# Kernel tuning notes

Hardware: AMD Instinct MI355X
Metric: run time of the kernel (lower is better)

The kernel has to match this reference:

```python
import jax, jax.numpy as jnp
import numpy as np

COST_KEYPOINT = 1.0
COST_GIOU = 1.0


def box_cxcyczwhd_to_xyzxyz(b):
    c, s = b[..., :3], b[..., 3:]
    return jnp.concatenate([c - 0.5 * s, c + 0.5 * s], axis=-1)


def generalized_3d_box_iou(b1, b2):
    # b1: [N,6], b2: [M,6], both xyzxyz. Returns [N,M] GIoU.
    vol1 = jnp.prod(b1[:, 3:] - b1[:, :3], axis=-1)
    vol2 = jnp.prod(b2[:, 3:] - b2[:, :3], axis=-1)
    lt = jnp.maximum(b1[:, None, :3], b2[None, :, :3])
    rb = jnp.minimum(b1[:, None, 3:], b2[None, :, 3:])
    inter = jnp.prod(jnp.maximum(rb - lt, 0.0), axis=-1)
    union = vol1[:, None] + vol2[None, :] - inter
    iou = inter / union
    elt = jnp.minimum(b1[:, None, :3], b2[None, :, :3])
    erb = jnp.maximum(b1[:, None, 3:], b2[None, :, 3:])
    evol = jnp.prod(jnp.maximum(erb - elt, 0.0), axis=-1)
    return iou - (evol - union) / evol


@jax.jit
def compute_cost(pred_keypoints, pred_boxes, tgt_boxes, tgt_keypoints):
    bs, Q = pred_keypoints.shape[:2]
    out_kp = pred_keypoints.reshape(bs * Q, -1)            # [bs*Q, K*3]
    out_boxes = pred_boxes.reshape(bs * Q, 6)
    tgt_b = tgt_boxes.reshape(-1, 6)                        # [T_total, 6]
    tgt_kp = tgt_keypoints.reshape(tgt_b.shape[0], -1)      # [T_total, K*3]
    xyz_min = box_cxcyczwhd_to_xyzxyz(tgt_b)[:, :3]
    K3 = tgt_kp.shape[-1]
    kp = tgt_kp.reshape(-1, K3 // 3, 3)
    # normalize keypoints relative to box min-corner and box size
    dist_kp = ((kp - xyz_min[:, None, :]) / tgt_b[:, None, 3:]).reshape(-1, K3)
    # L1 cdist: [bs*Q, T_total]
    cost_kp = jnp.sum(jnp.abs(out_kp[:, None, :] - dist_kp[None, :, :]), axis=-1)
    cost_giou = -generalized_3d_box_iou(
        box_cxcyczwhd_to_xyzxyz(out_boxes), box_cxcyczwhd_to_xyzxyz(tgt_b))
    C = COST_KEYPOINT * cost_kp + COST_GIOU * cost_giou
    return C.reshape(bs, Q, -1)


def _lap(cost):
    # Jonker-Volgenant shortest-augmenting-path LAP (scipy-style).
    # cost: [n, m] with n <= m. Returns (arange(n), col4row).
    cost = np.asarray(cost, dtype=np.float64)
    n, m = cost.shape
    u = np.zeros(n)
    v = np.zeros(m)
    col4row = np.full(n, -1, np.int64)
    row4col = np.full(m, -1, np.int64)
    for curRow in range(n):
        path = np.full(m, -1, np.int64)
        SR = np.zeros(n, bool)
        SC = np.zeros(m, bool)
        shortest = np.full(m, np.inf)
        minVal = 0.0
        i = curRow
        sink = -1
        while sink == -1:
            SR[i] = True
            idx = np.where(~SC)[0]
            r = minVal + cost[i, idx] - u[i] - v[idx]
            better = r < shortest[idx]
            shortest[idx[better]] = r[better]
            path[idx[better]] = i
            jloc = np.argmin(shortest[idx])
            j = idx[jloc]
            minVal = shortest[j]
            SC[j] = True
            if row4col[j] == -1:
                sink = j
            else:
                i = row4col[j]
        u[curRow] += minVal
        mask = SR.copy()
        mask[curRow] = False
        u[mask] += minVal - shortest[col4row[mask]]
        v[SC] -= minVal - shortest[SC]
        j = sink
        while True:
            i = path[j]
            row4col[j] = i
            col4row[i], j = j, col4row[i]
            if i == curRow:
                break
    return np.arange(n), col4row


def _linear_sum_assignment(cost):
    # cost: [Q, T] with Q >= T; mirrors scipy's transpose handling:
    # returns (row_ind sorted ascending, matching col_ind).
    rows, cols = _lap(cost.T)  # rows = arange(T) targets, cols = query ids
    order = np.argsort(cols)
    return cols[order], rows[order]


def setup_inputs() -> dict:
    key = jax.random.key(0)
    k1, k2, k3, k4, k5, k6 = jax.random.split(key, 6)
    BS, Q, T, K = 16, 300, 50, 17
    pred_keypoints = jax.random.normal(k1, (BS, Q, K * 3), dtype=jnp.float32)
    pred_boxes = jnp.concatenate([
        jax.random.uniform(k2, (BS, Q, 3), dtype=jnp.float32),
        jax.random.uniform(k3, (BS, Q, 3), dtype=jnp.float32) * 0.5 + 0.05,
    ], axis=-1)
    tgt_boxes = jnp.concatenate([
        jax.random.uniform(k4, (BS, T, 3), dtype=jnp.float32),
        jax.random.uniform(k5, (BS, T, 3), dtype=jnp.float32) * 0.5 + 0.05,
    ], axis=-1)
    tgt_keypoints = jax.random.uniform(k6, (BS, T, K * 3), dtype=jnp.float32)
    return {"pred_keypoints": pred_keypoints, "pred_boxes": pred_boxes,
            "tgt_boxes": tgt_boxes, "tgt_keypoints": tgt_keypoints}


def reference(pred_keypoints, pred_boxes, tgt_boxes, tgt_keypoints):
    C = compute_cost(pred_keypoints, pred_boxes, tgt_boxes, tgt_keypoints)
    Cn = np.asarray(C)
    bs, Q, _ = Cn.shape
    T = tgt_boxes.shape[1]
    # per-image block of the column-split cost matrix, as in torch C.split(sizes, -1)
    idx = []
    for b in range(bs):
        i, j = _linear_sum_assignment(Cn[b, :, b * T:(b + 1) * T])
        idx.append(np.stack([i, j]))
    indices = jnp.asarray(np.stack(idx), dtype=jnp.int32)  # [bs, 2, T]
    return C, indices
```

## Files before the change

kernel.cpp:

```cpp
#include <hip/hip_runtime.h>
#include <math.h>

#define BSZ 16
#define NQ 300
#define NT 50
#define K3 51
#define NPRED (BSZ*NQ)
#define NTGT  (BSZ*NT)
#define NC    (NPRED*NTGT)
#define TSTRIDE 301
#define SMEMF 15232


template<int CTRL, int RMASK>
__device__ __forceinline__ double dpp_minstep_f64(double x) {
    long long bb = __double_as_longlong(x);
    int lo = (int)(bb & 0xFFFFFFFFll);
    int hi = (int)(bb >> 32);
    int mlo = __builtin_amdgcn_update_dpp(lo, lo, CTRL, RMASK, 0xF, false);
    int mhi = __builtin_amdgcn_update_dpp(hi, hi, CTRL, RMASK, 0xF, false);
    double other = __longlong_as_double(((long long)mhi << 32) | (long long)(unsigned)mlo);
    return fmin(x, other);
}
__device__ __forceinline__ double wave_min_f64(double x) {
    x = dpp_minstep_f64<0xB1, 0xF>(x);
    x = dpp_minstep_f64<0x4E, 0xF>(x);
    x = dpp_minstep_f64<0x141, 0xF>(x);
    x = dpp_minstep_f64<0x140, 0xF>(x);
    x = dpp_minstep_f64<0x142, 0xA>(x);
    x = dpp_minstep_f64<0x143, 0xC>(x);
    long long bb = __double_as_longlong(x);
    int lo = __builtin_amdgcn_readlane((int)(bb & 0xFFFFFFFFll), 63);
    int hi = __builtin_amdgcn_readlane((int)(bb >> 32), 63);
    return __longlong_as_double(((long long)hi << 32) | (long long)(unsigned)lo);
}
__device__ __forceinline__ double readlane_f64(double x, int lane) {
    long long bb = __double_as_longlong(x);
    int lo = __builtin_amdgcn_readlane((int)(bb & 0xFFFFFFFFll), lane);
    int hi = __builtin_amdgcn_readlane((int)(bb >> 32), lane);
    return __longlong_as_double(((long long)hi << 32) | (long long)(unsigned)lo);
}

__device__ __forceinline__ float giou_cost(
    float plt0, float plt1, float plt2, float prb0, float prb1, float prb2, float pvol,
    float tlt0, float tlt1, float tlt2, float trb0, float trb1, float trb2, float tvol)
{
    float inter = fmaxf(fminf(prb0,trb0) - fmaxf(plt0,tlt0), 0.f);
    inter *= fmaxf(fminf(prb1,trb1) - fmaxf(plt1,tlt1), 0.f);
    inter *= fmaxf(fminf(prb2,trb2) - fmaxf(plt2,tlt2), 0.f);
    float evol = fmaxf(fmaxf(prb0,trb0) - fminf(plt0,tlt0), 0.f);
    evol *= fmaxf(fmaxf(prb1,trb1) - fminf(plt1,tlt1), 0.f);
    evol *= fmaxf(fmaxf(prb2,trb2) - fminf(plt2,tlt2), 0.f);
    float uni = pvol + tvol - inter;
    return inter/uni - (evol - uni)/evol;
}

__global__ __launch_bounds__(1024) void fused_kernel(
    const float* __restrict__ pred_kp, const float* __restrict__ pred_boxes,
    const float* __restrict__ tgt_boxes, const float* __restrict__ tgt_kp,
    float* __restrict__ C, float* __restrict__ out_idx)
{
    __shared__ __align__(16) float smem[SMEMF];
    const int bid = blockIdx.x;
    const int tid = threadIdx.x;

    if (bid >= BSZ) {
        const int cb = bid - BSZ;
        const int pb = cb % 75, tb = cb / 75;
        const int p0 = pb * 64, t0 = tb * 80;
        float* s_dk   = smem;
        float* s_tbox = smem + 4480;
        float* s_pk   = smem + 5440;

        if (tid < 80) {
            const float* tb6 = tgt_boxes + (size_t)(t0 + tid) * 6;
            float c0=tb6[0], c1=tb6[1], c2=tb6[2], s0=tb6[3], s1=tb6[4], s2=tb6[5];
            float l0=c0-0.5f*s0, l1=c1-0.5f*s1, l2=c2-0.5f*s2;
            float r0=c0+0.5f*s0, r1=c1+0.5f*s1, r2=c2+0.5f*s2;
            float* tw = s_tbox + tid*12;
            tw[0]=l0; tw[1]=l1; tw[2]=l2; tw[3]=r0; tw[4]=r1; tw[5]=r2;
            tw[6]=(r0-l0)*(r1-l1)*(r2-l2);
            tw[9]=s0; tw[10]=s1; tw[11]=s2;
        }
        __syncthreads();
        for (int e = tid; e < 80*K3; e += 1024) {
            int t = e / K3; int c = e - t*K3; int d = c % 3;
            float kp = tgt_kp[(size_t)t0*K3 + e];
            s_dk[t*56 + c] = (kp - s_tbox[t*12 + d]) / s_tbox[t*12 + 9 + d];
        }
        for (int e = tid; e < 64*K3; e += 1024)
            s_pk[e] = pred_kp[(size_t)p0*K3 + e];
        __syncthreads();

        const int pl = tid & 63, g = tid >> 6;
        float a[K3];
        #pragma unroll
        for (int c = 0; c < K3; ++c) a[c] = s_pk[pl*K3 + c];
        const int p = p0 + pl;
        const float* pb6 = pred_boxes + (size_t)p * 6;
        float pc0=pb6[0],pc1=pb6[1],pc2=pb6[2],ps0=pb6[3],ps1=pb6[4],ps2=pb6[5];
        float plt0=pc0-0.5f*ps0, plt1=pc1-0.5f*ps1, plt2=pc2-0.5f*ps2;
        float prb0=pc0+0.5f*ps0, prb1=pc1+0.5f*ps1, prb2=pc2+0.5f*ps2;
        float pvol=(prb0-plt0)*(prb1-plt1)*(prb2-plt2);

        #pragma unroll
        for (int k = 0; k < 5; ++k) {
            int tl = g*5 + k;
            const float* bbp = s_dk + tl*56;
            float sum = 0.f;
            #pragma unroll
            for (int c4 = 0; c4 < 12; ++c4) {
                float4 q = *(const float4*)(bbp + 4*c4);
                sum += fabsf(a[4*c4+0] - q.x);
                sum += fabsf(a[4*c4+1] - q.y);
                sum += fabsf(a[4*c4+2] - q.z);
                sum += fabsf(a[4*c4+3] - q.w);
            }
            sum += fabsf(a[48] - bbp[48]);
            sum += fabsf(a[49] - bbp[49]);
            sum += fabsf(a[50] - bbp[50]);
            const float* tw = s_tbox + tl*12;
            float g_ = giou_cost(plt0,plt1,plt2,prb0,prb1,prb2,pvol,
                                 tw[0],tw[1],tw[2],tw[3],tw[4],tw[5],tw[6]);
            C[(size_t)p*NTGT + (t0+tl)] = sum - g_;
        }
        return;
    }

    const int b = bid;
    const int ln = tid & 63, w = tid >> 6;
    const int bq0 = b*NQ, bt0 = b*NT;
    float* tile = smem;

    for (int e = tid; e < NT*K3; e += 1024)
        tile[e] = tgt_kp[(size_t)bt0*K3 + e];
    __syncthreads();

    float dk[K3];
    float tl0=0,tl1=0,tl2=0,tr0=0,tr1=0,tr2=0,tvol=0;
    if (ln < NT) {
        const float* tb6 = tgt_boxes + (size_t)(bt0+ln)*6;
        float c0=tb6[0],c1=tb6[1],c2=tb6[2],s0=tb6[3],s1=tb6[4],s2=tb6[5];
        tl0=c0-0.5f*s0; tl1=c1-0.5f*s1; tl2=c2-0.5f*s2;
        tr0=c0+0.5f*s0; tr1=c1+0.5f*s1; tr2=c2+0.5f*s2;
        tvol=(tr0-tl0)*(tr1-tl1)*(tr2-tl2);
        #pragma unroll
        for (int c = 0; c < K3; ++c) {
            int d = c % 3;
            float L = (d==0)?tl0:((d==1)?tl1:tl2);
            float S = (d==0)?s0:((d==1)?s1:s2);
            dk[c] = (tile[ln*K3 + c] - L) / S;
        }
    }
    __syncthreads();

    for (int p = w; p < NQ; p += 16) {
        const float* prow = pred_kp + (size_t)(bq0+p)*K3;
        const float* pb6  = pred_boxes + (size_t)(bq0+p)*6;
        float pc0=pb6[0],pc1=pb6[1],pc2=pb6[2],ps0=pb6[3],ps1=pb6[4],ps2=pb6[5];
        float plt0=pc0-0.5f*ps0, plt1=pc1-0.5f*ps1, plt2=pc2-0.5f*ps2;
        float prb0=pc0+0.5f*ps0, prb1=pc1+0.5f*ps1, prb2=pc2+0.5f*ps2;
        float pvol=(prb0-plt0)*(prb1-plt1)*(prb2-plt2);
        if (ln < NT) {
            float sum = 0.f;
            #pragma unroll
            for (int c = 0; c < K3; ++c) sum += fabsf(prow[c] - dk[c]);
            float g_ = giou_cost(plt0,plt1,plt2,prb0,prb1,prb2,pvol,
                                 tl0,tl1,tl2,tr0,tr1,tr2,tvol);
            tile[ln*TSTRIDE + p] = sum - g_;
        }
    }
    __syncthreads();

    float* s_rmv = smem + 15072;
    int*   s_rmc = (int*)(smem + 15136);
    for (int r = w; r < NT; r += 16) {
        float bv = __builtin_inff(); int bj = 0x7fffffff;
        #pragma unroll
        for (int s = 0; s < 5; ++s) {
            int j = ln + 64*s;
            if (j < NQ) {
                float cv = tile[r*TSTRIDE + j];
                if (cv < bv || (cv == bv && j < bj)) { bv = cv; bj = j; }
            }
        }
        #pragma unroll
        for (int off = 32; off > 0; off >>= 1) {
            float ov = __shfl_xor(bv, off);
            int   oj = __shfl_xor(bj, off);
            if (ov < bv || (ov == bv && oj < bj)) { bv = ov; bj = oj; }
        }
        if (ln == 0) { s_rmv[r] = bv; s_rmc[r] = bj; }
    }
    __syncthreads();
    if (w != 0) return;

    double u = 0.0;
    int c4r = -1;
    if (ln < NT) u = (double)s_rmv[ln];
    int wantj = (ln < NT) ? s_rmc[ln] : -1;
    for (int r = 0; r < NT; ++r) {
        int j = __builtin_amdgcn_readlane(wantj, r);
        unsigned long long taken = __ballot((ln < NT) && (c4r == j));
        if (taken == 0ull && ln == r) c4r = j;
    }

    double v[5], sh[5];
    int pth[5];
    #pragma unroll
    for (int s = 0; s < 5; ++s) v[s] = 0.0;
    const double DINF = __builtin_inf();

    for (int curRow = 0; curRow < NT; ++curRow) {
        if (__builtin_amdgcn_readlane(c4r, curRow) >= 0) continue;
        #pragma unroll
        for (int s = 0; s < 5; ++s) { sh[s] = DINF; pth[s] = -1; }
        int SCm = (ln < 44) ? 0 : 0x10;
        unsigned long long SRmask = 0ull;
        int i = curRow;
        double minVal = 0.0;
        int sink = -1;

        while (true) {
            SRmask |= (1ull << i);
            float cf[5];
            #pragma unroll
            for (int s = 0; s < 5; ++s) cf[s] = tile[i*TSTRIDE + ln + 64*s];
            double u_i = readlane_f64(u, i);
            double e[5];
            #pragma unroll
            for (int s = 0; s < 5; ++s) {
                bool open = ((SCm >> s) & 1) == 0;
                double r = ((minVal + (double)cf[s]) - u_i) - v[s];
                bool upd = open && (r < sh[s]);
                sh[s]  = upd ? r : sh[s];
                pth[s] = upd ? i : pth[s];
                e[s] = open ? sh[s] : DINF;
            }
            double lmin = fmin(fmin(fmin(e[0], e[1]), fmin(e[2], e[3])), e[4]);
            double m = wave_min_f64(lmin);
            minVal = m;
            unsigned long long b0 = __ballot((((SCm >> 0) & 1) == 0) && (sh[0] == m));
            unsigned long long b1 = __ballot((((SCm >> 1) & 1) == 0) && (sh[1] == m));
            unsigned long long b2 = __ballot((((SCm >> 2) & 1) == 0) && (sh[2] == m));
            unsigned long long b3 = __ballot((((SCm >> 3) & 1) == 0) && (sh[3] == m));
            unsigned long long b4 = __ballot((((SCm >> 4) & 1) == 0) && (sh[4] == m));
            int jstar;
            if      (b0) jstar =       __builtin_ctzll(b0);
            else if (b1) jstar =  64 + __builtin_ctzll(b1);
            else if (b2) jstar = 128 + __builtin_ctzll(b2);
            else if (b3) jstar = 192 + __builtin_ctzll(b3);
            else         jstar = 256 + __builtin_ctzll(b4);
            unsigned long long mm = __ballot((ln < NT) && (c4r == jstar));
            if (ln == (jstar & 63)) SCm |= 1 << (jstar >> 6);
            if (mm == 0ull) { sink = jstar; break; }
            i = __builtin_ctzll(mm);
        }

        int cg  = (c4r >= 0) ? c4r : 0;
        int gow = cg & 63, gsl = cg >> 6;
        double g0 = __shfl(sh[0], gow);
        double g1 = __shfl(sh[1], gow);
        double g2 = __shfl(sh[2], gow);
        double g3 = __shfl(sh[3], gow);
        double g4 = __shfl(sh[4], gow);
        double gg = g0;
        gg = (gsl == 1) ? g1 : gg;
        gg = (gsl == 2) ? g2 : gg;
        gg = (gsl == 3) ? g3 : gg;
        gg = (gsl == 4) ? g4 : gg;
        bool inSR = (ln < NT) && ((SRmask >> ln) & 1ull);
        double du = (ln == curRow) ? minVal : (minVal - gg);
        u = inSR ? (u + du) : u;
        #pragma unroll
        for (int s = 0; s < 5; ++s) {
            bool closed = ((SCm >> s) & 1) != 0;
            v[s] = closed ? (v[s] - (minVal - sh[s])) : v[s];
        }

        int j = sink;
        while (true) {
            int ow2 = j & 63, sl2 = j >> 6;
            int ps = pth[0];
            ps = (sl2==1) ? pth[1] : ps;
            ps = (sl2==2) ? pth[2] : ps;
            ps = (sl2==3) ? pth[3] : ps;
            ps = (sl2==4) ? pth[4] : ps;
            int ii = __builtin_amdgcn_readlane(ps, ow2);
            int jj = __builtin_amdgcn_readlane(c4r, ii);
            if (ln == ii) c4r = j;
            j = jj;
            if (ii == curRow) break;
        }
    }

    int* smem_i = (int*)smem;
    __threadfence_block();
    if (ln < NT) smem_i[ln] = c4r;
    __threadfence_block();
    int myc = c4r;
    int rank = 0;
    for (int s2 = 0; s2 < NT; ++s2) rank += (smem_i[s2] < myc) ? 1 : 0;
    if (ln < NT) {
        out_idx[b*(2*NT) + rank]      = (float)myc;
        out_idx[b*(2*NT) + NT + rank] = (float)ln;
    }
}

extern "C" void kernel_launch(void* const* d_in, const int* in_sizes, int n_in,
                              void* d_out, int out_size, void* d_ws, size_t ws_size,
                              hipStream_t stream)
{
    const float* pred_kp    = (const float*)d_in[0];
    const float* pred_boxes = (const float*)d_in[1];
    const float* tgt_boxes  = (const float*)d_in[2];
    const float* tgt_kp     = (const float*)d_in[3];
    float* C   = (float*)d_out;
    float* idx = C + NC;
    fused_kernel<<<dim3(BSZ + 750), 1024, 0, stream>>>(
        pred_kp, pred_boxes, tgt_boxes, tgt_kp, C, idx);
}
```

Before: 129.5 us.

## Add auction-style augmenting row reduction before shortest-path LAP phase

Inserts a bounded augmenting row reduction pass, as in the Jonker-Volgenant algorithm, ahead of the shortest-augmenting-path loop. Each free row finds its best and second-best reduced costs with wave-wide minima, lowers the price of the best column, and takes that column, evicting any previous owner. This is meant to leave fewer unassigned rows for the more expensive Dijkstra-style augmentation. In exchange it adds serial wave reductions and ballots per bid, and it must keep the dual variables consistent so the final assignment stays optimal.

```diff
diff --git a/kernel.cpp b/kernel.cpp
--- a/kernel.cpp
+++ b/kernel.cpp
@@ -210,6 +210,50 @@
     #pragma unroll
     for (int s = 0; s < 5; ++s) v[s] = 0.0;
     const double DINF = __builtin_inf();
+
+    {
+        int bidcnt = 0;
+        for (int steps = 0; steps < 200; ++steps) {
+            unsigned long long elig = __ballot((ln < NT) && (c4r == -1) && (bidcnt < 2));
+            if (!elig) break;
+            int i = __builtin_ctzll(elig);
+            if (ln == i) ++bidcnt;
+            float cf[5];
+            #pragma unroll
+            for (int s = 0; s < 5; ++s) cf[s] = tile[i*TSTRIDE + ln + 64*s];
+            double d[5];
+            #pragma unroll
+            for (int s = 0; s < 5; ++s)
+                d[s] = ((ln + 64*s) < NQ) ? ((double)cf[s] - v[s]) : DINF;
+            double l1 = fmin(fmin(fmin(d[0],d[1]), fmin(d[2],d[3])), d[4]);
+            double m1 = wave_min_f64(l1);
+            unsigned long long a0 = __ballot(d[0] == m1);
+            unsigned long long a1 = __ballot(d[1] == m1);
+            unsigned long long a2 = __ballot(d[2] == m1);
+            unsigned long long a3 = __ballot(d[3] == m1);
+            unsigned long long a4 = __ballot(d[4] == m1);
+            int j1;
+            if      (a0) j1 =       __builtin_ctzll(a0);
+            else if (a1) j1 =  64 + __builtin_ctzll(a1);
+            else if (a2) j1 = 128 + __builtin_ctzll(a2);
+            else if (a3) j1 = 192 + __builtin_ctzll(a3);
+            else         j1 = 256 + __builtin_ctzll(a4);
+            const int jsl = j1 >> 6;
+            const bool mine = (ln == (j1 & 63));
+            double t0_ = (mine && jsl == 0) ? DINF : d[0];
+            double t1_ = (mine && jsl == 1) ? DINF : d[1];
+            double t2_ = (mine && jsl == 2) ? DINF : d[2];
+            double t3_ = (mine && jsl == 3) ? DINF : d[3];
+            double t4_ = (mine && jsl == 4) ? DINF : d[4];
+            double l2 = fmin(fmin(fmin(t0_,t1_), fmin(t2_,t3_)), t4_);
+            double m2 = wave_min_f64(l2);
+            if (mine && (m1 < m2)) v[jsl] = v[jsl] - (m2 - m1);
+            if (ln == i) u = m2;
+            unsigned long long own = __ballot((ln < NT) && (c4r == j1));
+            if (ln == i) c4r = j1;
+            if (own != 0ull && ln == __builtin_ctzll(own)) c4r = -1;
+        }
+    }
 
     for (int curRow = 0; curRow < NT; ++curRow) {
         if (__builtin_amdgcn_readlane(c4r, curRow) >= 0) continue;
```

Measured after the change: 135.1 us. 4.3% more time.
